# Optimization experiments

Hardware: AMD Instinct MI355X
Metric: run time of the kernel (lower is better)

Reference implementation:

```python
import jax, jax.numpy as jnp
import numpy as np

H1 = 51  # lstm1 hidden size
H2 = 1   # lstm2 hidden size


def _lstm_cell(x, h, c, Wih, Whh, bih, bhh):
    # PyTorch LSTMCell: gates = x W_ih^T + b_ih + h W_hh^T + b_hh, order i,f,g,o
    gates = x @ Wih.T + h @ Whh.T + (bih + bhh)
    i, f, g, o = jnp.split(gates, 4, axis=-1)
    i = jax.nn.sigmoid(i)
    f = jax.nn.sigmoid(f)
    g = jnp.tanh(g)
    o = jax.nn.sigmoid(o)
    c_new = f * c + i * g
    h_new = o * jnp.tanh(c_new)
    return h_new, c_new


def setup_inputs() -> dict:
    key = jax.random.key(0)
    ks = jax.random.split(key, 9)
    B, T = 2048, 1024
    s1 = 1.0 / np.sqrt(H1)
    s2 = 1.0 / np.sqrt(H2)
    u = lambda k, shape, s: jax.random.uniform(k, shape, jnp.float32, -s, s)
    return {
        "input": jax.random.normal(ks[0], (B, T), dtype=jnp.float32),
        "W_ih1": u(ks[1], (4 * H1, 1), s1),
        "W_hh1": u(ks[2], (4 * H1, H1), s1),
        "b_ih1": u(ks[3], (4 * H1,), s1),
        "b_hh1": u(ks[4], (4 * H1,), s1),
        "W_ih2": u(ks[5], (4 * H2, H1), s2),
        "W_hh2": u(ks[6], (4 * H2, H2), s2),
        "b_ih2": u(ks[7], (4 * H2,), s2),
        "b_hh2": u(ks[8], (4 * H2,), s2),
        "future": 64,
    }


def reference(input, W_ih1, W_hh1, b_ih1, b_hh1, W_ih2, W_hh2, b_ih2, b_hh2, future):
    B = input.shape[0]
    dt = input.dtype
    h1 = jnp.zeros((B, H1), dt)
    c1 = jnp.zeros((B, H1), dt)
    h2 = jnp.zeros((B, H2), dt)
    c2 = jnp.zeros((B, H2), dt)

    def step(carry, x_t):
        h1, c1, h2, c2 = carry
        h1, c1 = _lstm_cell(x_t, h1, c1, W_ih1, W_hh1, b_ih1, b_hh1)
        h2, c2 = _lstm_cell(h1, h2, c2, W_ih2, W_hh2, b_ih2, b_hh2)
        return (h1, c1, h2, c2), h2

    xs = jnp.swapaxes(input, 0, 1)[:, :, None]  # [T, B, 1]
    carry, outs = jax.lax.scan(step, (h1, c1, h2, c2), xs)

    def step_future(carry, _):
        h1, c1, h2, c2 = carry
        h1, c1 = _lstm_cell(h2, h1, c1, W_ih1, W_hh1, b_ih1, b_hh1)
        h2, c2 = _lstm_cell(h1, h2, c2, W_ih2, W_hh2, b_ih2, b_hh2)
        return (h1, c1, h2, c2), h2

    if future > 0:
        _, outs_f = jax.lax.scan(step_future, carry, None, length=future)
        outs = jnp.concatenate([outs, outs_f], axis=0)

    # [T+F, B, 1] -> [B, T+F]
    return jnp.swapaxes(outs[:, :, 0], 0, 1)
```

## Files before the change

kernel.cpp:

```cpp
#include <hip/hip_runtime.h>


#define H1N  51
#define NP   26
#define WAVE 64

typedef float v2f __attribute__((ext_vector_type(2)));

#define INV_LN2   1.44269504088896340736f
#define INV_LN2X2 2.88539008177792681472f

__device__ __forceinline__ float sigmoid_s(float xs) {
    return __builtin_amdgcn_rcpf(1.0f + __builtin_amdgcn_exp2f(-xs));
}
__device__ __forceinline__ float tanh_s2(float xs2) {
    float e = __builtin_amdgcn_exp2f(xs2);
    return fmaf(-2.0f, __builtin_amdgcn_rcpf(e + 1.0f), 1.0f);
}
__device__ __forceinline__ float tanh_nat(float x) {
    return tanh_s2(x * INV_LN2X2);
}
__device__ __forceinline__ float rdlane(float v, int k) {
    return __int_as_float(__builtin_amdgcn_readlane(__float_as_int(v), k));
}

__global__ __attribute__((amdgpu_flat_work_group_size(64, 64),
                          amdgpu_waves_per_eu(1, 1)))
void lstm_seq2(const float* __restrict__ input,
               const float* __restrict__ W_ih1,
               const float* __restrict__ W_hh1,
               const float* __restrict__ b_ih1,
               const float* __restrict__ b_hh1,
               const float* __restrict__ W_ih2,
               const float* __restrict__ W_hh2,
               const float* __restrict__ b_ih2,
               const float* __restrict__ b_hh2,
               float* __restrict__ out,
               int T, int TF)
{
    const int j   = threadIdx.x;
    const bool jv = (j < H1N);
    const int jj  = jv ? j : 0;
    const float m = jv ? 1.0f : 0.0f;
    const bool isz = (j >= H1N) && (j < H1N + 4);
    const int  q   = isz ? (j - H1N) : 0;
    const float mz = isz ? 1.0f : 0.0f;
    const float s2q = (q == 2) ? INV_LN2X2 : INV_LN2;

    const int sA = 2 * blockIdx.x, sB = sA + 1;

    const int r_i = jj, r_f = H1N + jj, r_g = 2*H1N + jj, r_o = 3*H1N + jj;
    const float s_i = INV_LN2, s_f = INV_LN2, s_g = INV_LN2X2, s_o = INV_LN2;

    v2f wI[NP], wF[NP], wG[NP], wO[NP];
#pragma unroll
    for (int kk = 0; kk < NP; ++kk) {
        const int k0 = 2*kk, k1 = k0 + 1;
        wI[kk].x = m*s_i*W_hh1[r_i*H1N + k0] + mz*s2q*W_ih2[q*H1N + k0];
        wF[kk].x = m*s_f*W_hh1[r_f*H1N + k0];
        wG[kk].x = m*s_g*W_hh1[r_g*H1N + k0];
        wO[kk].x = m*s_o*W_hh1[r_o*H1N + k0];
        if (k1 < H1N) {
            wI[kk].y = m*s_i*W_hh1[r_i*H1N + k1] + mz*s2q*W_ih2[q*H1N + k1];
            wF[kk].y = m*s_f*W_hh1[r_f*H1N + k1];
            wG[kk].y = m*s_g*W_hh1[r_g*H1N + k1];
            wO[kk].y = m*s_o*W_hh1[r_o*H1N + k1];
        } else {
            wI[kk].y = m*s_i*(b_ih1[r_i] + b_hh1[r_i]);
            wF[kk].y = m*s_f*(b_ih1[r_f] + b_hh1[r_f]);
            wG[kk].y = m*s_g*(b_ih1[r_g] + b_hh1[r_g]);
            wO[kk].y = m*s_o*(b_ih1[r_o] + b_hh1[r_o]);
        }
    }
    const float wx_i = m*s_i*W_ih1[r_i];
    const float wx_f = m*s_f*W_ih1[r_f];
    const float wx_g = m*s_g*W_ih1[r_g];
    const float wx_o = m*s_o*W_ih1[r_o];

    const float wh2_0 = INV_LN2*W_hh2[0], wh2_1 = INV_LN2*W_hh2[1];
    const float wh2_2 = INV_LN2X2*W_hh2[2], wh2_3 = INV_LN2*W_hh2[3];
    const float b2_0 = INV_LN2*(b_ih2[0] + b_hh2[0]), b2_1 = INV_LN2*(b_ih2[1] + b_hh2[1]);
    const float b2_2 = INV_LN2X2*(b_ih2[2] + b_hh2[2]), b2_3 = INV_LN2*(b_ih2[3] + b_hh2[3]);

    __shared__ __align__(16) float hrowA[WAVE];
    __shared__ __align__(16) float hrowB[WAVE];
    __shared__ __align__(16) float2 zbuf[4];
    hrowA[j] = (j == H1N) ? 1.0f : 0.0f;
    hrowB[j] = (j == H1N) ? 1.0f : 0.0f;

    float h1A = 0.0f, c1A = 0.0f, h2A = 0.0f, c2A = 0.0f;
    float h1B = 0.0f, c1B = 0.0f, h2B = 0.0f, c2B = 0.0f;

    const float* __restrict__ xrowA = input + (long)sA * T;
    const float* __restrict__ xrowB = input + (long)sB * T;
    float* __restrict__ orowA = out + (long)sA * TF;
    float* __restrict__ orowB = out + (long)sB * TF;

    float xbufA = 0.0f, xbufB = 0.0f, obufA = 0.0f, obufB = 0.0f;

    for (int n = 0; n <= TF; ++n) {
        v2f aIA = {0.0f, 0.0f}, aFA = {0.0f, 0.0f};
        v2f aGA = {0.0f, 0.0f}, aOA = {0.0f, 0.0f};
        v2f aIB = {0.0f, 0.0f}, aFB = {0.0f, 0.0f};
        v2f aGB = {0.0f, 0.0f}, aOB = {0.0f, 0.0f};
#pragma unroll
        for (int kk = 0; kk < NP; ++kk) {
            const v2f hpA = *(const v2f*)&hrowA[2*kk];
            const v2f hpB = *(const v2f*)&hrowB[2*kk];
            asm("v_pk_fma_f32 %0, %8,  %12, %0\n\t"
                "v_pk_fma_f32 %4, %8,  %13, %4\n\t"
                "v_pk_fma_f32 %1, %9,  %12, %1\n\t"
                "v_pk_fma_f32 %5, %9,  %13, %5\n\t"
                "v_pk_fma_f32 %2, %10, %12, %2\n\t"
                "v_pk_fma_f32 %6, %10, %13, %6\n\t"
                "v_pk_fma_f32 %3, %11, %12, %3\n\t"
                "v_pk_fma_f32 %7, %11, %13, %7"
                : "+v"(aIA), "+v"(aFA), "+v"(aGA), "+v"(aOA),
                  "+v"(aIB), "+v"(aFB), "+v"(aGB), "+v"(aOB),
                  "+v"(wI[kk]), "+v"(wF[kk]), "+v"(wG[kk]), "+v"(wO[kk])
                : "v"(hpA), "v"(hpB));
        }
        const float mIA = aIA.x + aIA.y, mIB = aIB.x + aIB.y;
        if (isz) zbuf[q] = make_float2(mIA, mIB);
        const float mFA = aFA.x + aFA.y, mFB = aFB.x + aFB.y;
        const float mGA = aGA.x + aGA.y, mGB = aGB.x + aGB.y;
        const float mOA = aOA.x + aOA.y, mOB = aOB.x + aOB.y;

        if (n > 0) {
            const float2 z0 = zbuf[0], z1 = zbuf[1], z2 = zbuf[2], z3 = zbuf[3];
            {
                const float g2i = sigmoid_s(fmaf(wh2_0, h2A, b2_0 + z0.x));
                const float g2f = sigmoid_s(fmaf(wh2_1, h2A, b2_1 + z1.x));
                const float g2g = tanh_s2 (fmaf(wh2_2, h2A, b2_2 + z2.x));
                const float g2o = sigmoid_s(fmaf(wh2_3, h2A, b2_3 + z3.x));
                c2A = fmaf(g2f, c2A, g2i * g2g);
                h2A = g2o * tanh_nat(c2A);
            }
            {
                const float g2i = sigmoid_s(fmaf(wh2_0, h2B, b2_0 + z0.y));
                const float g2f = sigmoid_s(fmaf(wh2_1, h2B, b2_1 + z1.y));
                const float g2g = tanh_s2 (fmaf(wh2_2, h2B, b2_2 + z2.y));
                const float g2o = sigmoid_s(fmaf(wh2_3, h2B, b2_3 + z3.y));
                c2B = fmaf(g2f, c2B, g2i * g2g);
                h2B = g2o * tanh_nat(c2B);
            }
            const int tt = n - 1;
            if (j == (tt & 63)) { obufA = h2A; obufB = h2B; }
            if ((tt & 63) == 63) {
                orowA[tt - 63 + j] = obufA;
                orowB[tt - 63 + j] = obufB;
            }
        }

        if (n < TF) {
            float xA, xB;
            if (n < T) {
                if ((n & 63) == 0) { xbufA = xrowA[n + j]; xbufB = xrowB[n + j]; }
                xA = rdlane(xbufA, n & 63);
                xB = rdlane(xbufB, n & 63);
            } else {
                xA = h2A;
                xB = h2B;
            }
            {
                const float gi = sigmoid_s(fmaf(wx_i, xA, mIA));
                const float gf = sigmoid_s(fmaf(wx_f, xA, mFA));
                const float gg = tanh_s2 (fmaf(wx_g, xA, mGA));
                const float go = sigmoid_s(fmaf(wx_o, xA, mOA));
                c1A = fmaf(gf, c1A, gi * gg);
                h1A = go * tanh_nat(c1A);
            }
            {
                const float gi = sigmoid_s(fmaf(wx_i, xB, mIB));
                const float gf = sigmoid_s(fmaf(wx_f, xB, mFB));
                const float gg = tanh_s2 (fmaf(wx_g, xB, mGB));
                const float go = sigmoid_s(fmaf(wx_o, xB, mOB));
                c1B = fmaf(gf, c1B, gi * gg);
                h1B = go * tanh_nat(c1B);
            }
            if (jv) { hrowA[j] = h1A; hrowB[j] = h1B; }
        }
    }
}

extern "C" void kernel_launch(void* const* d_in, const int* in_sizes, int n_in,
                              void* d_out, int out_size, void* d_ws, size_t ws_size,
                              hipStream_t stream) {
    const float* input = (const float*)d_in[0];
    const float* W_ih1 = (const float*)d_in[1];
    const float* W_hh1 = (const float*)d_in[2];
    const float* b_ih1 = (const float*)d_in[3];
    const float* b_hh1 = (const float*)d_in[4];
    const float* W_ih2 = (const float*)d_in[5];
    const float* W_hh2 = (const float*)d_in[6];
    const float* b_ih2 = (const float*)d_in[7];
    const float* b_hh2 = (const float*)d_in[8];
    float* out = (float*)d_out;

    const int B  = 2048;
    const int T  = in_sizes[0] / B;
    const int TF = out_size   / B;

    lstm_seq2<<<dim3(B / 2), dim3(WAVE), 0, stream>>>(
        input, W_ih1, W_hh1, b_ih1, b_hh1, W_ih2, W_hh2, b_ih2, b_hh2,
        out, T, TF);
}
```

Baseline: 1.290 ms.

## Split per-step work into sequential per-sequence phases and peel loop edges

Each time step now runs as two separate phases, one per sequence. Each phase does its own matvec, layer-2 cell and layer-1 cell, so one sequence's LDS round trip can overlap the other's math, instead of both sequences' matvecs being fused in one asm block. The prologue, the input-driven steps, the future steps and the final step are peeled into separate loops, which removes the per-iteration n>0/n<TF/n<T branches. It also adds an empty asm barrier to pin the weight registers and splits the z buffer per sequence so it is read as a float4. Output flushing is reorganized, and it assumes T and TF are multiples of 64.

Result: no change. 1.275 ms (-1.2%).

```diff
diff --git a/kernel.cpp b/kernel.cpp
--- a/kernel.cpp
+++ b/kernel.cpp
@@ -72,6 +72,10 @@
             wO[kk].y = m*s_o*(b_ih1[r_o] + b_hh1[r_o]);
         }
     }
+#pragma unroll
+    for (int kk = 0; kk < NP; ++kk)
+        asm volatile("" : "+v"(wI[kk]), "+v"(wF[kk]), "+v"(wG[kk]), "+v"(wO[kk]));
+
     const float wx_i = m*s_i*W_ih1[r_i];
     const float wx_f = m*s_f*W_ih1[r_f];
     const float wx_g = m*s_g*W_ih1[r_g];
@@ -84,12 +88,13 @@
 
     __shared__ __align__(16) float hrowA[WAVE];
     __shared__ __align__(16) float hrowB[WAVE];
-    __shared__ __align__(16) float2 zbuf[4];
+    __shared__ __align__(16) float zbA[4];
+    __shared__ __align__(16) float zbB[4];
     hrowA[j] = (j == H1N) ? 1.0f : 0.0f;
     hrowB[j] = (j == H1N) ? 1.0f : 0.0f;
 
-    float h1A = 0.0f, c1A = 0.0f, h2A = 0.0f, c2A = 0.0f;
-    float h1B = 0.0f, c1B = 0.0f, h2B = 0.0f, c2B = 0.0f;
+    float c1A = 0.0f, h2A = 0.0f, c2A = 0.0f;
+    float c1B = 0.0f, h2B = 0.0f, c2B = 0.0f;
 
     const float* __restrict__ xrowA = input + (long)sA * T;
     const float* __restrict__ xrowB = input + (long)sB * T;
@@ -98,89 +103,78 @@
 
     float xbufA = 0.0f, xbufB = 0.0f, obufA = 0.0f, obufB = 0.0f;
 
-    for (int n = 0; n <= TF; ++n) {
-        v2f aIA = {0.0f, 0.0f}, aFA = {0.0f, 0.0f};
-        v2f aGA = {0.0f, 0.0f}, aOA = {0.0f, 0.0f};
-        v2f aIB = {0.0f, 0.0f}, aFB = {0.0f, 0.0f};
-        v2f aGB = {0.0f, 0.0f}, aOB = {0.0f, 0.0f};
+    auto phase = [&](int sel, float& c1, float& h2, float& c2, float& obuf,
+                     float xin, int xmode, int do_l2, int do_fin, int tt) {
+        float* hrow = sel ? hrowB : hrowA;
+        float* zb   = sel ? zbB   : zbA;
+        v2f aI = {0.0f, 0.0f}, aF = {0.0f, 0.0f};
+        v2f aG = {0.0f, 0.0f}, aO = {0.0f, 0.0f};
 #pragma unroll
         for (int kk = 0; kk < NP; ++kk) {
-            const v2f hpA = *(const v2f*)&hrowA[2*kk];
-            const v2f hpB = *(const v2f*)&hrowB[2*kk];
-            asm("v_pk_fma_f32 %0, %8,  %12, %0\n\t"
-                "v_pk_fma_f32 %4, %8,  %13, %4\n\t"
-                "v_pk_fma_f32 %1, %9,  %12, %1\n\t"
-                "v_pk_fma_f32 %5, %9,  %13, %5\n\t"
-                "v_pk_fma_f32 %2, %10, %12, %2\n\t"
-                "v_pk_fma_f32 %6, %10, %13, %6\n\t"
-                "v_pk_fma_f32 %3, %11, %12, %3\n\t"
-                "v_pk_fma_f32 %7, %11, %13, %7"
-                : "+v"(aIA), "+v"(aFA), "+v"(aGA), "+v"(aOA),
-                  "+v"(aIB), "+v"(aFB), "+v"(aGB), "+v"(aOB),
-                  "+v"(wI[kk]), "+v"(wF[kk]), "+v"(wG[kk]), "+v"(wO[kk])
-                : "v"(hpA), "v"(hpB));
-        }
-        const float mIA = aIA.x + aIA.y, mIB = aIB.x + aIB.y;
-        if (isz) zbuf[q] = make_float2(mIA, mIB);
-        const float mFA = aFA.x + aFA.y, mFB = aFB.x + aFB.y;
-        const float mGA = aGA.x + aGA.y, mGB = aGB.x + aGB.y;
-        const float mOA = aOA.x + aOA.y, mOB = aOB.x + aOB.y;
-
-        if (n > 0) {
-            const float2 z0 = zbuf[0], z1 = zbuf[1], z2 = zbuf[2], z3 = zbuf[3];
-            {
-                const float g2i = sigmoid_s(fmaf(wh2_0, h2A, b2_0 + z0.x));
-                const float g2f = sigmoid_s(fmaf(wh2_1, h2A, b2_1 + z1.x));
-                const float g2g = tanh_s2 (fmaf(wh2_2, h2A, b2_2 + z2.x));
-                const float g2o = sigmoid_s(fmaf(wh2_3, h2A, b2_3 + z3.x));
-                c2A = fmaf(g2f, c2A, g2i * g2g);
-                h2A = g2o * tanh_nat(c2A);
-            }
-            {
-                const float g2i = sigmoid_s(fmaf(wh2_0, h2B, b2_0 + z0.y));
-                const float g2f = sigmoid_s(fmaf(wh2_1, h2B, b2_1 + z1.y));
-                const float g2g = tanh_s2 (fmaf(wh2_2, h2B, b2_2 + z2.y));
-                const float g2o = sigmoid_s(fmaf(wh2_3, h2B, b2_3 + z3.y));
-                c2B = fmaf(g2f, c2B, g2i * g2g);
-                h2B = g2o * tanh_nat(c2B);
-            }
-            const int tt = n - 1;
-            if (j == (tt & 63)) { obufA = h2A; obufB = h2B; }
-            if ((tt & 63) == 63) {
-                orowA[tt - 63 + j] = obufA;
-                orowB[tt - 63 + j] = obufB;
-            }
-        }
-
-        if (n < TF) {
-            float xA, xB;
-            if (n < T) {
-                if ((n & 63) == 0) { xbufA = xrowA[n + j]; xbufB = xrowB[n + j]; }
-                xA = rdlane(xbufA, n & 63);
-                xB = rdlane(xbufB, n & 63);
-            } else {
-                xA = h2A;
-                xB = h2B;
-            }
-            {
-                const float gi = sigmoid_s(fmaf(wx_i, xA, mIA));
-                const float gf = sigmoid_s(fmaf(wx_f, xA, mFA));
-                const float gg = tanh_s2 (fmaf(wx_g, xA, mGA));
-                const float go = sigmoid_s(fmaf(wx_o, xA, mOA));
-                c1A = fmaf(gf, c1A, gi * gg);
-                h1A = go * tanh_nat(c1A);
-            }
-            {
-                const float gi = sigmoid_s(fmaf(wx_i, xB, mIB));
-                const float gf = sigmoid_s(fmaf(wx_f, xB, mFB));
-                const float gg = tanh_s2 (fmaf(wx_g, xB, mGB));
-                const float go = sigmoid_s(fmaf(wx_o, xB, mOB));
-                c1B = fmaf(gf, c1B, gi * gg);
-                h1B = go * tanh_nat(c1B);
-            }
-            if (jv) { hrowA[j] = h1A; hrowB[j] = h1B; }
+            const v2f hp = *(const v2f*)&hrow[2*kk];
+            asm("v_pk_fma_f32 %0, %4, %8, %0\n\t"
+                "v_pk_fma_f32 %1, %5, %8, %1\n\t"
+                "v_pk_fma_f32 %2, %6, %8, %2\n\t"
+                "v_pk_fma_f32 %3, %7, %8, %3"
+                : "+v"(aI), "+v"(aF), "+v"(aG), "+v"(aO)
+                : "v"(wI[kk]), "v"(wF[kk]), "v"(wG[kk]), "v"(wO[kk]), "v"(hp));
+        }
+        const float mI = aI.x + aI.y;
+        if (isz) zb[q] = mI;
+        const float mF = aF.x + aF.y, mG = aG.x + aG.y, mO = aO.x + aO.y;
+
+        if (do_l2) {
+            const float4 z = *(const float4*)zb;
+            const float g2i = sigmoid_s(fmaf(wh2_0, h2, b2_0 + z.x));
+            const float g2f = sigmoid_s(fmaf(wh2_1, h2, b2_1 + z.y));
+            const float g2g = tanh_s2 (fmaf(wh2_2, h2, b2_2 + z.z));
+            const float g2o = sigmoid_s(fmaf(wh2_3, h2, b2_3 + z.w));
+            c2 = fmaf(g2f, c2, g2i * g2g);
+            h2 = g2o * tanh_nat(c2);
+            obuf = (j == (tt & 63)) ? h2 : obuf;
+        }
+        if (do_fin) {
+            const float x = (xmode == 0) ? xin : h2;
+            const float gi = sigmoid_s(fmaf(wx_i, x, mI));
+            const float gf = sigmoid_s(fmaf(wx_f, x, mF));
+            const float gg = tanh_s2 (fmaf(wx_g, x, mG));
+            const float go = sigmoid_s(fmaf(wx_o, x, mO));
+            c1 = fmaf(gf, c1, gi * gg);
+            const float h1 = go * tanh_nat(c1);
+            if (jv) hrow[j] = h1;
+        }
+    };
+
+    xbufA = xrowA[j]; xbufB = xrowB[j];
+    phase(0, c1A, h2A, c2A, obufA, rdlane(xbufA, 0), 0, 0, 1, 0);
+    phase(1, c1B, h2B, c2B, obufB, rdlane(xbufB, 0), 0, 0, 1, 0);
+
+    for (int n = 1; n < T; ++n) {
+        if ((n & 63) == 0) { xbufA = xrowA[n + j]; xbufB = xrowB[n + j]; }
+        const int u = n & 63;
+        const float xA = rdlane(xbufA, u), xB = rdlane(xbufB, u);
+        phase(0, c1A, h2A, c2A, obufA, xA, 0, 1, 1, n - 1);
+        phase(1, c1B, h2B, c2B, obufB, xB, 0, 1, 1, n - 1);
+        if ((n & 63) == 0) {
+            orowA[n - 64 + j] = obufA;
+            orowB[n - 64 + j] = obufB;
         }
     }
+
+    phase(0, c1A, h2A, c2A, obufA, 0.0f, 1, 1, 1, T - 1);
+    phase(1, c1B, h2B, c2B, obufB, 0.0f, 1, 1, 1, T - 1);
+    orowA[T - 64 + j] = obufA;
+    orowB[T - 64 + j] = obufB;
+
+    for (int n = T + 1; n < TF; ++n) {
+        phase(0, c1A, h2A, c2A, obufA, 0.0f, 1, 1, 1, n - 1);
+        phase(1, c1B, h2B, c2B, obufB, 0.0f, 1, 1, 1, n - 1);
+    }
+
+    phase(0, c1A, h2A, c2A, obufA, 0.0f, 1, 1, 0, TF - 1);
+    phase(1, c1B, h2B, c2B, obufB, 0.0f, 1, 1, 0, TF - 1);
+    orowA[TF - 64 + j] = obufA;
+    orowB[TF - 64 + j] = obufB;
 }
 
 extern "C" void kernel_launch(void* const* d_in, const int* in_sizes, int n_in,
```

## Split LSTM gate rows across two waves per block with LDS gate exchange

Applied to the files above, without the earlier changes.

Each block now runs two waves for the same pair of sequences. Wave 0 computes the input and forget gates and wave 1 computes the cell and output gates, so each wave holds half the weight registers and does half the recurrent matvec per step. The waves swap activated gate values through shared memory and two __syncthreads barriers per timestep, then both update the cell state redundantly. The loop is also peeled into specialised phases (first step, input steps, future steps, final step) to drop per-step branches. The aim is to shorten the serial per-step critical path and hide latency by running two waves per SIMD, at the cost of barrier and LDS traffic on every step.

Result: slower. 1.469 ms (+13.9%).

```diff
diff --git a/kernel.cpp b/kernel.cpp
--- a/kernel.cpp
+++ b/kernel.cpp
@@ -24,58 +24,60 @@
     return __int_as_float(__builtin_amdgcn_readlane(__float_as_int(v), k));
 }
 
-__global__ __attribute__((amdgpu_flat_work_group_size(64, 64),
-                          amdgpu_waves_per_eu(1, 1)))
-void lstm_seq2(const float* __restrict__ input,
-               const float* __restrict__ W_ih1,
-               const float* __restrict__ W_hh1,
-               const float* __restrict__ b_ih1,
-               const float* __restrict__ b_hh1,
-               const float* __restrict__ W_ih2,
-               const float* __restrict__ W_hh2,
-               const float* __restrict__ b_ih2,
-               const float* __restrict__ b_hh2,
-               float* __restrict__ out,
-               int T, int TF)
+__global__ __attribute__((amdgpu_flat_work_group_size(128, 128),
+                          amdgpu_waves_per_eu(2, 2)))
+void lstm_gs(const float* __restrict__ input,
+             const float* __restrict__ W_ih1,
+             const float* __restrict__ W_hh1,
+             const float* __restrict__ b_ih1,
+             const float* __restrict__ b_hh1,
+             const float* __restrict__ W_ih2,
+             const float* __restrict__ W_hh2,
+             const float* __restrict__ b_ih2,
+             const float* __restrict__ b_hh2,
+             float* __restrict__ out,
+             int T, int TF)
 {
-    const int j   = threadIdx.x;
+    const int tid = threadIdx.x;
+    const int wv  = tid >> 6;
+    const int j   = tid & (WAVE - 1);
     const bool jv = (j < H1N);
     const int jj  = jv ? j : 0;
     const float m = jv ? 1.0f : 0.0f;
-    const bool isz = (j >= H1N) && (j < H1N + 4);
+    const bool isz = (wv == 0) && (j >= H1N) && (j < H1N + 4);
     const int  q   = isz ? (j - H1N) : 0;
     const float mz = isz ? 1.0f : 0.0f;
     const float s2q = (q == 2) ? INV_LN2X2 : INV_LN2;
 
     const int sA = 2 * blockIdx.x, sB = sA + 1;
 
-    const int r_i = jj, r_f = H1N + jj, r_g = 2*H1N + jj, r_o = 3*H1N + jj;
-    const float s_i = INV_LN2, s_f = INV_LN2, s_g = INV_LN2X2, s_o = INV_LN2;
-
-    v2f wI[NP], wF[NP], wG[NP], wO[NP];
+    const int rX = (wv ? 2 : 0) * H1N + jj;
+    const int rY = (wv ? 3 : 1) * H1N + jj;
+    const float sX = wv ? INV_LN2X2 : INV_LN2;
+    const float sY = INV_LN2;
+    const float scX = wv ? 2.0f : 1.0f;
+    const float ofX = wv ? -1.0f : 0.0f;
+
+    v2f wX[NP], wY[NP];
 #pragma unroll
     for (int kk = 0; kk < NP; ++kk) {
         const int k0 = 2*kk, k1 = k0 + 1;
-        wI[kk].x = m*s_i*W_hh1[r_i*H1N + k0] + mz*s2q*W_ih2[q*H1N + k0];
-        wF[kk].x = m*s_f*W_hh1[r_f*H1N + k0];
-        wG[kk].x = m*s_g*W_hh1[r_g*H1N + k0];
-        wO[kk].x = m*s_o*W_hh1[r_o*H1N + k0];
+        wX[kk].x = m*sX*W_hh1[rX*H1N + k0] + mz*s2q*W_ih2[q*H1N + k0];
+        wY[kk].x = m*sY*W_hh1[rY*H1N + k0];
         if (k1 < H1N) {
-            wI[kk].y = m*s_i*W_hh1[r_i*H1N + k1] + mz*s2q*W_ih2[q*H1N + k1];
-            wF[kk].y = m*s_f*W_hh1[r_f*H1N + k1];
-            wG[kk].y = m*s_g*W_hh1[r_g*H1N + k1];
-            wO[kk].y = m*s_o*W_hh1[r_o*H1N + k1];
+            wX[kk].y = m*sX*W_hh1[rX*H1N + k1] + mz*s2q*W_ih2[q*H1N + k1];
+            wY[kk].y = m*sY*W_hh1[rY*H1N + k1];
         } else {
-            wI[kk].y = m*s_i*(b_ih1[r_i] + b_hh1[r_i]);
-            wF[kk].y = m*s_f*(b_ih1[r_f] + b_hh1[r_f]);
-            wG[kk].y = m*s_g*(b_ih1[r_g] + b_hh1[r_g]);
-            wO[kk].y = m*s_o*(b_ih1[r_o] + b_hh1[r_o]);
+            wX[kk].y = m*sX*(b_ih1[rX] + b_hh1[rX]);
+            wY[kk].y = m*sY*(b_ih1[rY] + b_hh1[rY]);
         }
     }
-    const float wx_i = m*s_i*W_ih1[r_i];
-    const float wx_f = m*s_f*W_ih1[r_f];
-    const float wx_g = m*s_g*W_ih1[r_g];
-    const float wx_o = m*s_o*W_ih1[r_o];
+#pragma unroll
+    for (int kk = 0; kk < NP; ++kk)
+        asm volatile("" : "+v"(wX[kk]), "+v"(wY[kk]));
+
+    const float wxX = m*sX*W_ih1[rX];
+    const float wxY = m*sY*W_ih1[rY];
 
     const float wh2_0 = INV_LN2*W_hh2[0], wh2_1 = INV_LN2*W_hh2[1];
     const float wh2_2 = INV_LN2X2*W_hh2[2], wh2_3 = INV_LN2*W_hh2[3];
@@ -84,103 +86,100 @@
 
     __shared__ __align__(16) float hrowA[WAVE];
     __shared__ __align__(16) float hrowB[WAVE];
-    __shared__ __align__(16) float2 zbuf[4];
+    __shared__ __align__(16) float2 zAB[4];
+    __shared__ __align__(16) float2 gex[2][2][WAVE];
     hrowA[j] = (j == H1N) ? 1.0f : 0.0f;
     hrowB[j] = (j == H1N) ? 1.0f : 0.0f;
-
-    float h1A = 0.0f, c1A = 0.0f, h2A = 0.0f, c2A = 0.0f;
-    float h1B = 0.0f, c1B = 0.0f, h2B = 0.0f, c2B = 0.0f;
+    __syncthreads();
+
+    float c1A = 0.0f, c1B = 0.0f;
+    float h2A = 0.0f, c2A = 0.0f, h2B = 0.0f, c2B = 0.0f;
 
     const float* __restrict__ xrowA = input + (long)sA * T;
     const float* __restrict__ xrowB = input + (long)sB * T;
-    float* __restrict__ orowA = out + (long)sA * TF;
-    float* __restrict__ orowB = out + (long)sB * TF;
-
-    float xbufA = 0.0f, xbufB = 0.0f, obufA = 0.0f, obufB = 0.0f;
-
-    for (int n = 0; n <= TF; ++n) {
-        v2f aIA = {0.0f, 0.0f}, aFA = {0.0f, 0.0f};
-        v2f aGA = {0.0f, 0.0f}, aOA = {0.0f, 0.0f};
-        v2f aIB = {0.0f, 0.0f}, aFB = {0.0f, 0.0f};
-        v2f aGB = {0.0f, 0.0f}, aOB = {0.0f, 0.0f};
+    float* __restrict__ orow = out + (long)(wv ? sB : sA) * TF;
+
+    float xbufA = 0.0f, xbufB = 0.0f, obuf = 0.0f;
+
+    auto iter = [&](int n, int DO_L2, int DO_FIN, int XMODE) {
+        v2f aXA = {0.0f, 0.0f}, aYA = {0.0f, 0.0f};
+        v2f aXB = {0.0f, 0.0f}, aYB = {0.0f, 0.0f};
 #pragma unroll
         for (int kk = 0; kk < NP; ++kk) {
             const v2f hpA = *(const v2f*)&hrowA[2*kk];
             const v2f hpB = *(const v2f*)&hrowB[2*kk];
-            asm("v_pk_fma_f32 %0, %8,  %12, %0\n\t"
-                "v_pk_fma_f32 %4, %8,  %13, %4\n\t"
-                "v_pk_fma_f32 %1, %9,  %12, %1\n\t"
-                "v_pk_fma_f32 %5, %9,  %13, %5\n\t"
-                "v_pk_fma_f32 %2, %10, %12, %2\n\t"
-                "v_pk_fma_f32 %6, %10, %13, %6\n\t"
-                "v_pk_fma_f32 %3, %11, %12, %3\n\t"
-                "v_pk_fma_f32 %7, %11, %13, %7"
-                : "+v"(aIA), "+v"(aFA), "+v"(aGA), "+v"(aOA),
-                  "+v"(aIB), "+v"(aFB), "+v"(aGB), "+v"(aOB),
-                  "+v"(wI[kk]), "+v"(wF[kk]), "+v"(wG[kk]), "+v"(wO[kk])
-                : "v"(hpA), "v"(hpB));
-        }
-        const float mIA = aIA.x + aIA.y, mIB = aIB.x + aIB.y;
-        if (isz) zbuf[q] = make_float2(mIA, mIB);
-        const float mFA = aFA.x + aFA.y, mFB = aFB.x + aFB.y;
-        const float mGA = aGA.x + aGA.y, mGB = aGB.x + aGB.y;
-        const float mOA = aOA.x + aOA.y, mOB = aOB.x + aOB.y;
-
-        if (n > 0) {
-            const float2 z0 = zbuf[0], z1 = zbuf[1], z2 = zbuf[2], z3 = zbuf[3];
+            asm("v_pk_fma_f32 %0, %4, %6, %0\n\t"
+                "v_pk_fma_f32 %1, %5, %6, %1\n\t"
+                "v_pk_fma_f32 %2, %4, %7, %2\n\t"
+                "v_pk_fma_f32 %3, %5, %7, %3"
+                : "+v"(aXA), "+v"(aYA), "+v"(aXB), "+v"(aYB)
+                : "v"(wX[kk]), "v"(wY[kk]), "v"(hpA), "v"(hpB));
+        }
+        const float sXA = aXA.x + aXA.y, sYA = aYA.x + aYA.y;
+        const float sXB = aXB.x + aXB.y, sYB = aYB.x + aYB.y;
+        if (isz) zAB[q] = make_float2(sXA, sXB);
+        __syncthreads();
+
+        if (DO_L2) {
+            const float4 zp0 = *(const float4*)&zAB[0];
+            const float4 zp1 = *(const float4*)&zAB[2];
             {
-                const float g2i = sigmoid_s(fmaf(wh2_0, h2A, b2_0 + z0.x));
-                const float g2f = sigmoid_s(fmaf(wh2_1, h2A, b2_1 + z1.x));
-                const float g2g = tanh_s2 (fmaf(wh2_2, h2A, b2_2 + z2.x));
-                const float g2o = sigmoid_s(fmaf(wh2_3, h2A, b2_3 + z3.x));
+                const float g2i = sigmoid_s(fmaf(wh2_0, h2A, b2_0 + zp0.x));
+                const float g2f = sigmoid_s(fmaf(wh2_1, h2A, b2_1 + zp0.z));
+                const float g2g = tanh_s2 (fmaf(wh2_2, h2A, b2_2 + zp1.x));
+                const float g2o = sigmoid_s(fmaf(wh2_3, h2A, b2_3 + zp1.z));
                 c2A = fmaf(g2f, c2A, g2i * g2g);
                 h2A = g2o * tanh_nat(c2A);
             }
             {
-                const float g2i = sigmoid_s(fmaf(wh2_0, h2B, b2_0 + z0.y));
-                const float g2f = sigmoid_s(fmaf(wh2_1, h2B, b2_1 + z1.y));
-                const float g2g = tanh_s2 (fmaf(wh2_2, h2B, b2_2 + z2.y));
-                const float g2o = sigmoid_s(fmaf(wh2_3, h2B, b2_3 + z3.y));
+                const float g2i = sigmoid_s(fmaf(wh2_0, h2B, b2_0 + zp0.y));
+                const float g2f = sigmoid_s(fmaf(wh2_1, h2B, b2_1 + zp0.w));
+                const float g2g = tanh_s2 (fmaf(wh2_2, h2B, b2_2 + zp1.y));
+                const float g2o = sigmoid_s(fmaf(wh2_3, h2B, b2_3 + zp1.w));
                 c2B = fmaf(g2f, c2B, g2i * g2g);
                 h2B = g2o * tanh_nat(c2B);
             }
             const int tt = n - 1;
-            if (j == (tt & 63)) { obufA = h2A; obufB = h2B; }
-            if ((tt & 63) == 63) {
-                orowA[tt - 63 + j] = obufA;
-                orowB[tt - 63 + j] = obufB;
-            }
-        }
-
-        if (n < TF) {
+            const float h2mine = wv ? h2B : h2A;
+            if (j == (tt & 63)) obuf = h2mine;
+            if ((tt & 63) == 63) orow[tt - 63 + j] = obuf;
+        }
+
+        if (DO_FIN) {
             float xA, xB;
-            if (n < T) {
+            if (XMODE == 0) {
                 if ((n & 63) == 0) { xbufA = xrowA[n + j]; xbufB = xrowB[n + j]; }
                 xA = rdlane(xbufA, n & 63);
                 xB = rdlane(xbufB, n & 63);
             } else {
-                xA = h2A;
-                xB = h2B;
+                xA = h2A;  xB = h2B;
             }
-            {
-                const float gi = sigmoid_s(fmaf(wx_i, xA, mIA));
-                const float gf = sigmoid_s(fmaf(wx_f, xA, mFA));
-                const float gg = tanh_s2 (fmaf(wx_g, xA, mGA));
-                const float go = sigmoid_s(fmaf(wx_o, xA, mOA));
-                c1A = fmaf(gf, c1A, gi * gg);
-                h1A = go * tanh_nat(c1A);
-            }
-            {
-                const float gi = sigmoid_s(fmaf(wx_i, xB, mIB));
-                const float gf = sigmoid_s(fmaf(wx_f, xB, mFB));
-                const float gg = tanh_s2 (fmaf(wx_g, xB, mGB));
-                const float go = sigmoid_s(fmaf(wx_o, xB, mOB));
-                c1B = fmaf(gf, c1B, gi * gg);
-                h1B = go * tanh_nat(c1B);
-            }
+            const float gXA = fmaf(scX, sigmoid_s(fmaf(wxX, xA, sXA)), ofX);
+            const float gYA =            sigmoid_s(fmaf(wxY, xA, sYA));
+            const float gXB = fmaf(scX, sigmoid_s(fmaf(wxX, xB, sXB)), ofX);
+            const float gYB =            sigmoid_s(fmaf(wxY, xB, sYB));
+            gex[wv][0][j] = make_float2(gXA, gXB);
+            gex[wv][1][j] = make_float2(gYA, gYB);
+            __syncthreads();
+            const float2 oX = gex[1 - wv][0][j];
+            const float2 oY = gex[1 - wv][1][j];
+            const float iA = wv ? oX.x : gXA, fA = wv ? oY.x : gYA;
+            const float gA = wv ? gXA : oX.x, oA = wv ? gYA : oY.x;
+            const float iB = wv ? oX.y : gXB, fB = wv ? oY.y : gYB;
+            const float gB = wv ? gXB : oX.y, oB = wv ? gYB : oY.y;
+            c1A = fmaf(fA, c1A, iA * gA);
+            c1B = fmaf(fB, c1B, iB * gB);
+            const float h1A = oA * tanh_nat(c1A);
+            const float h1B = oB * tanh_nat(c1B);
             if (jv) { hrowA[j] = h1A; hrowB[j] = h1B; }
         }
-    }
+    };
+
+    iter(0, 0, 1, 0);
+    for (int n = 1; n < T; ++n) iter(n, 1, 1, 0);
+    iter(T, 1, 1, 1);
+    for (int n = T + 1; n < TF; ++n) iter(n, 1, 1, 1);
+    iter(TF, 1, 0, 1);
 }
 
 extern "C" void kernel_launch(void* const* d_in, const int* in_sizes, int n_in,
@@ -201,7 +200,7 @@
     const int T  = in_sizes[0] / B;
     const int TF = out_size   / B;
 
-    lstm_seq2<<<dim3(B / 2), dim3(WAVE), 0, stream>>>(
+    lstm_gs<<<dim3(B / 2), dim3(128), 0, stream>>>(
         input, W_ih1, W_hh1, b_ih1, b_hh1, W_ih2, W_hh2, b_ih2, b_hh2,
         out, T, TF);
 }
```
